# Optimization experiments

Measured on AMD Instinct MI355X. Metric: run time of the kernel, lower is better.

## Reference

```python
import jax, jax.numpy as jnp
import numpy as np
from jax import lax

K_SIZE = 5  # dilated_kernel_size


def dcls_kernel(w, p, k=K_SIZE):
    """Build dense (Cout,Cin,k,k) kernel from DCLS v1 bilinear interpolation.
    w: (Cout,Cin,Kc) weights; p: (2,Cout,Cin,Kc) learnable positions."""
    lim = k // 2
    pos = jnp.clip(p, -lim, lim) + lim          # in [0, k-1]
    i = jnp.floor(pos).astype(jnp.int32)
    r = pos - i                                  # bilinear fractions
    Co, Ci, Kc = w.shape
    co = jnp.arange(Co)[:, None, None]
    ci = jnp.arange(Ci)[None, :, None]
    i1, i2 = i[0], i[1]
    r1, r2 = r[0], r[1]
    # scatter into (k+1)x(k+1) grid so i+1 never goes out of bounds, then trim
    K = jnp.zeros((Co, Ci, k + 1, k + 1), w.dtype)
    K = K.at[co, ci, i1,     i2    ].add(w * (1 - r1) * (1 - r2))
    K = K.at[co, ci, i1 + 1, i2    ].add(w * r1 * (1 - r2))
    K = K.at[co, ci, i1,     i2 + 1].add(w * (1 - r1) * r2)
    K = K.at[co, ci, i1 + 1, i2 + 1].add(w * r1 * r2)
    return K[:, :, :k, :k]


def conv2d(x, K, pad):
    return lax.conv_general_dilated(
        x, K, window_strides=(1, 1), padding=[(pad, pad), (pad, pad)],
        dimension_numbers=('NCHW', 'OIHW', 'NCHW'))


def maxpool2(x):
    return lax.reduce_window(x, -jnp.inf, lax.max, (1, 1, 2, 2), (1, 1, 2, 2), 'VALID')


def setup_inputs() -> dict:
    key = jax.random.key(0)
    ks = jax.random.split(key, 12)
    lim = K_SIZE // 2
    B = 4096
    x = jax.random.normal(ks[0], (B, 1, 28, 28), jnp.float32)
    w1 = jax.random.normal(ks[1], (32, 1, 16), jnp.float32) * 0.2
    p1 = jax.random.uniform(ks[2], (2, 32, 1, 16), jnp.float32, -lim, lim)
    b1 = jnp.zeros((32,), jnp.float32)
    w2 = jax.random.normal(ks[3], (64, 32, 32), jnp.float32) * 0.05
    p2 = jax.random.uniform(ks[4], (2, 64, 32, 32), jnp.float32, -lim, lim)
    b2 = jnp.zeros((64,), jnp.float32)
    fc1_w = jax.random.normal(ks[5], (128, 64 * 7 * 7), jnp.float32) * 0.02
    fc1_b = jnp.zeros((128,), jnp.float32)
    fc2_w = jax.random.normal(ks[6], (10, 128), jnp.float32) * 0.08
    fc2_b = jnp.zeros((10,), jnp.float32)
    return dict(x=x, w1=w1, p1=p1, b1=b1, w2=w2, p2=p2, b2=b2,
                fc1_w=fc1_w, fc1_b=fc1_b, fc2_w=fc2_w, fc2_b=fc2_b)


def reference(x, w1, p1, b1, w2, p2, b2, fc1_w, fc1_b, fc2_w, fc2_b):
    h = conv2d(x, dcls_kernel(w1, p1), pad=2) + b1[None, :, None, None]
    h = maxpool2(jax.nn.relu(h))                       # (B,32,14,14)
    h = conv2d(h, dcls_kernel(w2, p2), pad=2) + b2[None, :, None, None]
    h = maxpool2(jax.nn.relu(h))                       # (B,64,7,7)
    h = h.reshape(-1, 64 * 7 * 7)
    h = jax.nn.relu(h @ fc1_w.T + fc1_b)
    return h @ fc2_w.T + fc2_b                         # (B,10)
```

## Files before the change

### kernel.cpp

```cpp
#include <hip/hip_runtime.h>
#include <hip/hip_bf16.h>

typedef __attribute__((ext_vector_type(8))) short short8;
typedef __attribute__((ext_vector_type(4))) short short4v;
typedef __attribute__((ext_vector_type(4))) float float4v;
typedef __attribute__((ext_vector_type(16))) float float16v;

static __device__ __forceinline__ unsigned short f2bf(float f) {
    unsigned u = __float_as_uint(f);
    unsigned r = (u + 0x7FFF + ((u >> 16) & 1)) >> 16;
    return (unsigned short)r;
}

__global__ __launch_bounds__(256) void prep_all(
    const float* __restrict__ w1, const float* __restrict__ p1,
    const float* __restrict__ w2, const float* __restrict__ p2,
    const float* __restrict__ fc1w,
    unsigned short* __restrict__ K1b,
    unsigned short* __restrict__ Kt,
    unsigned short* __restrict__ w1b) {
    const int blk = blockIdx.x;
    const int t = threadIdx.x;

    if (blk < 8) {
        int cell = blk * 256 + t;
        int co = cell >> 6;
        int k = cell & 63;
        int wr = k >> 3;
        int kx = k & 7;
        float acc = 0.f;
        if (wr < 5 && kx < 5) {
#pragma unroll 8
            for (int kc = 0; kc < 16; ++kc) {
                float wv = w1[co * 16 + kc];
                float pa = p1[co * 16 + kc];
                float pb = p1[512 + co * 16 + kc];
                float pos1 = fminf(fmaxf(pa, -2.f), 2.f) + 2.f;
                float pos2 = fminf(fmaxf(pb, -2.f), 2.f) + 2.f;
                int i1 = (int)floorf(pos1);
                int i2 = (int)floorf(pos2);
                float r1 = pos1 - (float)i1;
                float r2 = pos2 - (float)i2;
                float c = 0.f;
                if (i1 == wr && i2 == kx) c += (1.f - r1) * (1.f - r2);
                if (i1 + 1 == wr && i2 == kx) c += r1 * (1.f - r2);
                if (i1 == wr && i2 + 1 == kx) c += (1.f - r1) * r2;
                if (i1 + 1 == wr && i2 + 1 == kx) c += r1 * r2;
                acc += wv * c;
            }
        }
        K1b[cell] = f2bf(acc);
    } else if (blk < 208) {
        int cell = (blk - 8) * 256 + t;
        int kk = cell >> 11;
        int co = (cell >> 5) & 63;
        int ci = cell & 31;
        int ky = kk / 5;
        int kx = kk - 5 * ky;
        const int base = (co * 32 + ci) * 32;
        float acc = 0.f;
#pragma unroll 8
        for (int kc = 0; kc < 32; ++kc) {
            float wv = w2[base + kc];
            float pa = p2[base + kc];
            float pb = p2[65536 + base + kc];
            float pos1 = fminf(fmaxf(pa, -2.f), 2.f) + 2.f;
            float pos2 = fminf(fmaxf(pb, -2.f), 2.f) + 2.f;
            int i1 = (int)floorf(pos1);
            int i2 = (int)floorf(pos2);
            float r1 = pos1 - (float)i1;
            float r2 = pos2 - (float)i2;
            float c = 0.f;
            if (i1 == ky && i2 == kx) c += (1.f - r1) * (1.f - r2);
            if (i1 + 1 == ky && i2 == kx) c += r1 * (1.f - r2);
            if (i1 == ky && i2 + 1 == kx) c += (1.f - r1) * r2;
            if (i1 + 1 == ky && i2 + 1 == kx) c += r1 * r2;
            acc += wv * c;
        }
        int nt = co >> 5, mq = co & 31;
        int kh2 = ci >> 4, hh = (ci >> 3) & 1, jj = ci & 7;
        Kt[kk * 2048 + nt * 1024 + kh2 * 512 + hh * 256 + mq * 8 + jj] = f2bf(acc);
    } else {
        int i8 = ((blk - 208) * 256 + t) * 8;
        float4 v0 = *(const float4*)(fc1w + i8);
        float4 v1 = *(const float4*)(fc1w + i8 + 4);
        short8 o = {(short)f2bf(v0.x), (short)f2bf(v0.y), (short)f2bf(v0.z),
                    (short)f2bf(v0.w), (short)f2bf(v1.x), (short)f2bf(v1.y),
                    (short)f2bf(v1.z), (short)f2bf(v1.w)};
        *(short8*)(w1b + i8) = o;
    }
}

__global__ __launch_bounds__(256, 4) void fused_conv_mfma(
    const float* __restrict__ x,
    const unsigned short* __restrict__ K1b,
    const unsigned short* __restrict__ Kt,
    const float* __restrict__ b1,
    const float* __restrict__ b2,
    unsigned short* __restrict__ h2) {
    __shared__ __align__(16) unsigned short h1p[18 * 20 * 40];
    __shared__ __align__(16) unsigned short sm4[4 * 29 * 44];
    __shared__ __align__(16) unsigned short sm_xb[784];

    const int b = blockIdx.x;
    const int tid = threadIdx.x;
    const int lane = tid & 63;
    const int wv = tid >> 6;
    const int n16 = lane & 15;
    const int cig = lane >> 4;

    const int yi = 2 * (n16 >> 3) + ((n16 >> 1) & 1);
    const int xi = 2 * ((n16 >> 2) & 1) + (n16 & 1);
    const int pYo = cig >> 1, pXo = cig & 1;

    const int mq = lane & 31;
    const int Qx = mq >> 2;
    const int dy2 = (mq >> 1) & 1;
    const int dx2 = mq & 1;
    const int hh = lane >> 5;

    for (int t = tid; t < 1800; t += 256) ((uint4*)h1p)[t] = uint4{0, 0, 0, 0};
    {
        const float* xb = x + (size_t)b * 784;
        for (int t = tid; t < 784; t += 256) sm_xb[t] = f2bf(xb[t]);
    }
    __syncthreads();

    if (tid < 116) {
        int s = tid / 29;
        int r = tid - s * 29;
        unsigned short* dst = sm4 + (s * 29 + r) * 44;
        bool rok = r < 28;
#pragma unroll
        for (int g2 = 0; g2 < 11; ++g2) {
            short4v v;
#pragma unroll
            for (int e = 0; e < 4; ++e) {
                int c = g2 * 4 + e + s - 4;
                v[e] = (short)((rok && (unsigned)c < 28u) ? sm_xb[r * 28 + c]
                                                          : (unsigned short)0);
            }
            *(short4v*)(dst + g2 * 4) = v;
        }
    }

    short8 bw[2][2];
    float bias1[2], bias2n[2];
#pragma unroll
    for (int cot = 0; cot < 2; ++cot) {
#pragma unroll
        for (int h = 0; h < 2; ++h)
            bw[cot][h] = *(const short8*)(K1b + (cot * 16 + n16) * 64 + h * 32 + cig * 8);
        bias1[cot] = b1[cot * 16 + n16];
    }
#pragma unroll
    for (int nt = 0; nt < 2; ++nt) bias2n[nt] = b2[nt * 32 + mq];

    const int s1 = (xi + 2) & 3;
    const int pb1 = (xi + 2) & ~3;
    const unsigned short* a1base = sm4 + s1 * (29 * 44) + pb1;

    __syncthreads();

    for (int i = 0; i < 13; ++i) {
        int t = wv + 4 * i;
        if (t < 49) {
            int tY = t / 7, tX = t - 7 * tY;
            const unsigned short* ab = a1base + 4 * tX;
            int r0 = 4 * tY + yi - 2 + cig;
            int r1 = r0 + 4;
            int rr0 = ((unsigned)r0 < 28u) ? r0 : 28;
            int rr1 = ((unsigned)r1 < 28u) ? r1 : 28;
            short4v lo0 = *(const short4v*)(ab + rr0 * 44);
            short4v hi0 = *(const short4v*)(ab + rr0 * 44 + 4);
            short4v lo1 = *(const short4v*)(ab + rr1 * 44);
            short4v hi1 = *(const short4v*)(ab + rr1 * 44 + 4);
            short8 af0 = {lo0[0], lo0[1], lo0[2], lo0[3], hi0[0], hi0[1], hi0[2], hi0[3]};
            short8 af1 = {lo1[0], lo1[1], lo1[2], lo1[3], hi1[0], hi1[1], hi1[2], hi1[3]};
            int pY = 2 * tY + pYo, pX = 2 * tX + pXo;
#pragma unroll
            for (int cot = 0; cot < 2; ++cot) {
                float4v acc = {0.f, 0.f, 0.f, 0.f};
                acc = __builtin_amdgcn_mfma_f32_16x16x32_bf16(af0, bw[cot][0], acc, 0, 0, 0);
                acc = __builtin_amdgcn_mfma_f32_16x16x32_bf16(af1, bw[cot][1], acc, 0, 0, 0);
                float v = fmaxf(fmaxf(acc[0], acc[1]), fmaxf(acc[2], acc[3]));
                v = fmaxf(v + bias1[cot], 0.f);
                h1p[((pY + 2) * 20 + (pX + 2)) * 40 + cot * 16 + n16] = f2bf(v);
            }
        }
    }

    int x2 = 2 * Qx + dx2;
    if (x2 > 13) x2 = 13;
    int aoff00, aoff01, aoff10, aoff11;
    int pYv0, pYv1;
    {
        int pY0 = 2 * wv;
        int pY1 = 2 * wv + 1;
        int y20 = 2 * pY0 + dy2; if (y20 > 13) y20 = 13;
        int y21 = 2 * pY1 + dy2; if (y21 > 13) y21 = 13;
        pYv0 = pY0; pYv1 = pY1;
        aoff00 = (y20 * 20 + x2) * 40 + hh * 8;
        aoff01 = aoff00 + 16;
        aoff10 = (y21 * 20 + x2) * 40 + hh * 8;
        aoff11 = aoff10 + 16;
    }
    const unsigned short* KtL = Kt + lane * 8;

    float16v acc00, acc01, acc10, acc11;
#pragma unroll
    for (int e = 0; e < 16; ++e) { acc00[e] = 0.f; acc01[e] = 0.f; acc10[e] = 0.f; acc11[e] = 0.f; }

    __syncthreads();

#pragma unroll 1
    for (int ky = 0; ky < 5; ++ky) {
        const unsigned short* kbase = KtL + ky * 5 * 2048;
        const int sbase = ky * 20 * 40;
#pragma unroll
        for (int kx = 0; kx < 5; ++kx) {
            const unsigned short* kb = kbase + kx * 2048;
            const int soff = sbase + kx * 40;
            short8 wf00 = *(const short8*)(kb);
            short8 wf01 = *(const short8*)(kb + 512);
            short8 wf10 = *(const short8*)(kb + 1024);
            short8 wf11 = *(const short8*)(kb + 1536);
            short8 af00 = *(const short8*)(h1p + aoff00 + soff);
            short8 af01 = *(const short8*)(h1p + aoff01 + soff);
            short8 af10 = *(const short8*)(h1p + aoff10 + soff);
            short8 af11 = *(const short8*)(h1p + aoff11 + soff);
            acc00 = __builtin_amdgcn_mfma_f32_32x32x16_bf16(af00, wf00, acc00, 0, 0, 0);
            acc00 = __builtin_amdgcn_mfma_f32_32x32x16_bf16(af01, wf01, acc00, 0, 0, 0);
            acc01 = __builtin_amdgcn_mfma_f32_32x32x16_bf16(af00, wf10, acc01, 0, 0, 0);
            acc01 = __builtin_amdgcn_mfma_f32_32x32x16_bf16(af01, wf11, acc01, 0, 0, 0);
            acc10 = __builtin_amdgcn_mfma_f32_32x32x16_bf16(af10, wf00, acc10, 0, 0, 0);
            acc10 = __builtin_amdgcn_mfma_f32_32x32x16_bf16(af11, wf01, acc10, 0, 0, 0);
            acc11 = __builtin_amdgcn_mfma_f32_32x32x16_bf16(af10, wf10, acc11, 0, 0, 0);
            acc11 = __builtin_amdgcn_mfma_f32_32x32x16_bf16(af11, wf11, acc11, 0, 0, 0);
        }
    }

    unsigned short* outb = h2 + (size_t)b * 3136;
    if (pYv0 < 7) {
#pragma unroll
        for (int g2 = 0; g2 < 4; ++g2) {
            int pX = 2 * g2 + hh;
            if (pX < 7) {
                float v0 = fmaxf(fmaxf(acc00[4 * g2], acc00[4 * g2 + 1]),
                                 fmaxf(acc00[4 * g2 + 2], acc00[4 * g2 + 3]));
                v0 = fmaxf(v0 + bias2n[0], 0.f);
                outb[mq * 49 + pYv0 * 7 + pX] = f2bf(v0);
                float v1 = fmaxf(fmaxf(acc01[4 * g2], acc01[4 * g2 + 1]),
                                 fmaxf(acc01[4 * g2 + 2], acc01[4 * g2 + 3]));
                v1 = fmaxf(v1 + bias2n[1], 0.f);
                outb[(32 + mq) * 49 + pYv0 * 7 + pX] = f2bf(v1);
            }
        }
    }
    if (pYv1 < 7) {
#pragma unroll
        for (int g2 = 0; g2 < 4; ++g2) {
            int pX = 2 * g2 + hh;
            if (pX < 7) {
                float v0 = fmaxf(fmaxf(acc10[4 * g2], acc10[4 * g2 + 1]),
                                 fmaxf(acc10[4 * g2 + 2], acc10[4 * g2 + 3]));
                v0 = fmaxf(v0 + bias2n[0], 0.f);
                outb[mq * 49 + pYv1 * 7 + pX] = f2bf(v0);
                float v1 = fmaxf(fmaxf(acc11[4 * g2], acc11[4 * g2 + 1]),
                                 fmaxf(acc11[4 * g2 + 2], acc11[4 * g2 + 3]));
                v1 = fmaxf(v1 + bias2n[1], 0.f);
                outb[(32 + mq) * 49 + pYv1 * 7 + pX] = f2bf(v1);
            }
        }
    }
}

__global__ __launch_bounds__(256) void fc1_mfma(
    const unsigned short* __restrict__ A,
    const unsigned short* __restrict__ Wb,
    float* __restrict__ part, size_t PB) {
    __shared__ __align__(16) unsigned short As[64 * 72];
    const int blk = blockIdx.x;
    const int kh = blk % 7;
    const int m0 = (blk / 7) * 64;
    const int tid = threadIdx.x;
    const int wv = tid >> 6;
    const int lane = tid & 63;
    const int n16 = lane & 15;
    const int cig = lane >> 4;

    float4v acc[4][2];
#pragma unroll
    for (int mt = 0; mt < 4; ++mt)
#pragma unroll
        for (int j = 0; j < 2; ++j) acc[mt][j] = float4v{0.f, 0.f, 0.f, 0.f};

    for (int it = 0; it < 7; ++it) {
        int k0 = kh * 448 + it * 64;
        __syncthreads();
#pragma unroll
        for (int i = 0; i < 2; ++i) {
            int p = tid + 256 * i;
            int r = p >> 3, ko = (p & 7) * 8;
            *(short8*)(As + r * 72 + ko) =
                *(const short8*)(A + (size_t)(m0 + r) * 3136 + k0 + ko);
        }
        __syncthreads();
#pragma unroll
        for (int h = 0; h < 2; ++h) {
            short8 af[4];
#pragma unroll
            for (int mt = 0; mt < 4; ++mt)
                af[mt] = *(const short8*)(As + (mt * 16 + n16) * 72 + h * 32 + cig * 8);
            short8 wf[2];
#pragma unroll
            for (int j = 0; j < 2; ++j)
                wf[j] = *(const short8*)(Wb + (size_t)((wv * 2 + j) * 16 + n16) * 3136 +
                                         k0 + h * 32 + cig * 8);
#pragma unroll
            for (int mt = 0; mt < 4; ++mt)
#pragma unroll
                for (int j = 0; j < 2; ++j)
                    acc[mt][j] = __builtin_amdgcn_mfma_f32_16x16x32_bf16(
                        af[mt], wf[j], acc[mt][j], 0, 0, 0);
        }
    }
    float* o = part + (size_t)kh * PB;
#pragma unroll
    for (int mt = 0; mt < 4; ++mt)
#pragma unroll
        for (int j = 0; j < 2; ++j)
#pragma unroll
            for (int r = 0; r < 4; ++r) {
                int row = m0 + mt * 16 + cig * 4 + r;
                o[(size_t)row * 128 + (wv * 2 + j) * 16 + n16] = acc[mt][j][r];
            }
}

__global__ __launch_bounds__(256) void fc2_kernel(
    const float* __restrict__ part, size_t PB,
    const float* __restrict__ fc1b,
    const float* __restrict__ W, const float* __restrict__ bias,
    float* __restrict__ out) {
    __shared__ float smW[10 * 132];
    __shared__ float smB1[128];
    __shared__ float smB[10];
    int t = threadIdx.x;
    for (int i = t; i < 1280; i += 256) {
        int n = i >> 7, k = i & 127;
        smW[n * 132 + k] = W[i];
    }
    if (t < 128) smB1[t] = fc1b[t];
    if (t < 10) smB[t] = bias[t];
    __syncthreads();
    const int r = t >> 3;
    const int q = t & 7;
    const size_t b = (size_t)blockIdx.x * 32 + r;
    const float* pb = part + b * 128 + q * 16;

    float rv[16];
#pragma unroll
    for (int c = 0; c < 4; ++c) {
        float4 s = *(const float4*)(pb + 4 * c);
#pragma unroll
        for (int j = 1; j < 7; ++j) {
            float4 pj = *(const float4*)(pb + (size_t)j * PB + 4 * c);
            s.x += pj.x; s.y += pj.y; s.z += pj.z; s.w += pj.w;
        }
        float4 bv = *(const float4*)(smB1 + q * 16 + 4 * c);
        rv[4 * c + 0] = fmaxf(s.x + bv.x, 0.f);
        rv[4 * c + 1] = fmaxf(s.y + bv.y, 0.f);
        rv[4 * c + 2] = fmaxf(s.z + bv.z, 0.f);
        rv[4 * c + 3] = fmaxf(s.w + bv.w, 0.f);
    }
    float acc[10];
#pragma unroll
    for (int n = 0; n < 10; ++n) {
        const float4* wr = (const float4*)(smW + n * 132 + q * 16);
        float a = 0.f;
#pragma unroll
        for (int c = 0; c < 4; ++c) {
            float4 w = wr[c];
            a += rv[4 * c] * w.x + rv[4 * c + 1] * w.y +
                 rv[4 * c + 2] * w.z + rv[4 * c + 3] * w.w;
        }
        acc[n] = a;
    }
#pragma unroll
    for (int n = 0; n < 10; ++n) {
        acc[n] += __shfl_xor(acc[n], 1);
        acc[n] += __shfl_xor(acc[n], 2);
        acc[n] += __shfl_xor(acc[n], 4);
    }
    if (q == 0) {
#pragma unroll
        for (int n = 0; n < 10; ++n) out[b * 10 + n] = acc[n] + smB[n];
    }
}

extern "C" void kernel_launch(void* const* d_in, const int* in_sizes, int n_in,
                              void* d_out, int out_size, void* d_ws, size_t ws_size,
                              hipStream_t stream) {
    const float* x    = (const float*)d_in[0];
    const float* w1   = (const float*)d_in[1];
    const float* p1   = (const float*)d_in[2];
    const float* b1   = (const float*)d_in[3];
    const float* w2   = (const float*)d_in[4];
    const float* p2   = (const float*)d_in[5];
    const float* b2   = (const float*)d_in[6];
    const float* fc1w = (const float*)d_in[7];
    const float* fc1b = (const float*)d_in[8];
    const float* fc2w = (const float*)d_in[9];
    const float* fc2b = (const float*)d_in[10];
    float* out = (float*)d_out;

    const int B = in_sizes[0] / 784;

    float* ws = (float*)d_ws;
    unsigned short* Kt  = (unsigned short*)ws;
    unsigned short* K1b = (unsigned short*)(ws + 25600);
    unsigned short* w1b = (unsigned short*)(ws + 26624);
    unsigned short* h2b = (unsigned short*)(ws + 227328);
    float* fc1p = ws + 227328 + (size_t)B * 1568;

    prep_all<<<404, 256, 0, stream>>>(w1, p1, w2, p2, fc1w, K1b, Kt, w1b);
    fused_conv_mfma<<<B, 256, 0, stream>>>(x, K1b, Kt, b1, b2, h2b);
    fc1_mfma<<<(B / 64) * 7, 256, 0, stream>>>(h2b, w1b, fc1p, (size_t)B * 128);
    fc2_kernel<<<B / 32, 256, 0, stream>>>(fc1p, (size_t)B * 128,
                                           fc1b, fc2w, fc2b, out);
}
```

Before: 209.7 us.

## Process two images per block in fused conv to reuse conv2 weight loads

```diff
diff --git a/kernel.cpp b/kernel.cpp
--- a/kernel.cpp
+++ b/kernel.cpp
@@ -91,18 +91,19 @@
     }
 }
 
-__global__ __launch_bounds__(256, 4) void fused_conv_mfma(
+__global__ __launch_bounds__(256, 2) void fused_conv2(
     const float* __restrict__ x,
     const unsigned short* __restrict__ K1b,
     const unsigned short* __restrict__ Kt,
     const float* __restrict__ b1,
     const float* __restrict__ b2,
     unsigned short* __restrict__ h2) {
-    __shared__ __align__(16) unsigned short h1p[18 * 20 * 40];
+    __shared__ __align__(16) unsigned short h1pA[18 * 20 * 40];
+    __shared__ __align__(16) unsigned short h1pB[18 * 20 * 40];
     __shared__ __align__(16) unsigned short sm4[4 * 29 * 44];
     __shared__ __align__(16) unsigned short sm_xb[784];
 
-    const int b = blockIdx.x;
+    const int b0 = blockIdx.x * 2;
     const int tid = threadIdx.x;
     const int lane = tid & 63;
     const int wv = tid >> 6;
@@ -119,12 +120,29 @@
     const int dx2 = mq & 1;
     const int hh = lane >> 5;
 
-    for (int t = tid; t < 1800; t += 256) ((uint4*)h1p)[t] = uint4{0, 0, 0, 0};
+    for (int t = tid; t < 1800; t += 256) ((uint4*)h1pA)[t] = uint4{0, 0, 0, 0};
+    for (int t = tid; t < 1800; t += 256) ((uint4*)h1pB)[t] = uint4{0, 0, 0, 0};
     {
-        const float* xb = x + (size_t)b * 784;
+        const float* xb = x + (size_t)b0 * 784;
         for (int t = tid; t < 784; t += 256) sm_xb[t] = f2bf(xb[t]);
     }
     __syncthreads();
+
+    short8 bw[2][2];
+    float bias1[2], bias2n[2];
+#pragma unroll
+    for (int cot = 0; cot < 2; ++cot) {
+#pragma unroll
+        for (int h = 0; h < 2; ++h)
+            bw[cot][h] = *(const short8*)(K1b + (cot * 16 + n16) * 64 + h * 32 + cig * 8);
+        bias1[cot] = b1[cot * 16 + n16];
+    }
+#pragma unroll
+    for (int nt = 0; nt < 2; ++nt) bias2n[nt] = b2[nt * 32 + mq];
+
+    const int s1 = (xi + 2) & 3;
+    const int pb1 = (xi + 2) & ~3;
+    const unsigned short* a1base = sm4 + s1 * (29 * 44) + pb1;
 
     if (tid < 116) {
         int s = tid / 29;
@@ -143,23 +161,6 @@
             *(short4v*)(dst + g2 * 4) = v;
         }
     }
-
-    short8 bw[2][2];
-    float bias1[2], bias2n[2];
-#pragma unroll
-    for (int cot = 0; cot < 2; ++cot) {
-#pragma unroll
-        for (int h = 0; h < 2; ++h)
-            bw[cot][h] = *(const short8*)(K1b + (cot * 16 + n16) * 64 + h * 32 + cig * 8);
-        bias1[cot] = b1[cot * 16 + n16];
-    }
-#pragma unroll
-    for (int nt = 0; nt < 2; ++nt) bias2n[nt] = b2[nt * 32 + mq];
-
-    const int s1 = (xi + 2) & 3;
-    const int pb1 = (xi + 2) & ~3;
-    const unsigned short* a1base = sm4 + s1 * (29 * 44) + pb1;
-
     __syncthreads();
 
     for (int i = 0; i < 13; ++i) {
@@ -185,7 +186,59 @@
                 acc = __builtin_amdgcn_mfma_f32_16x16x32_bf16(af1, bw[cot][1], acc, 0, 0, 0);
                 float v = fmaxf(fmaxf(acc[0], acc[1]), fmaxf(acc[2], acc[3]));
                 v = fmaxf(v + bias1[cot], 0.f);
-                h1p[((pY + 2) * 20 + (pX + 2)) * 40 + cot * 16 + n16] = f2bf(v);
+                h1pA[((pY + 2) * 20 + (pX + 2)) * 40 + cot * 16 + n16] = f2bf(v);
+            }
+        }
+    }
+    {
+        const float* xb = x + ((size_t)b0 + 1) * 784;
+        for (int t = tid; t < 784; t += 256) sm_xb[t] = f2bf(xb[t]);
+    }
+    __syncthreads();
+
+    if (tid < 116) {
+        int s = tid / 29;
+        int r = tid - s * 29;
+        unsigned short* dst = sm4 + (s * 29 + r) * 44;
+        bool rok = r < 28;
+#pragma unroll
+        for (int g2 = 0; g2 < 11; ++g2) {
+            short4v v;
+#pragma unroll
+            for (int e = 0; e < 4; ++e) {
+                int c = g2 * 4 + e + s - 4;
+                v[e] = (short)((rok && (unsigned)c < 28u) ? sm_xb[r * 28 + c]
+                                                          : (unsigned short)0);
+            }
+            *(short4v*)(dst + g2 * 4) = v;
+        }
+    }
+    __syncthreads();
+
+    for (int i = 0; i < 13; ++i) {
+        int t = wv + 4 * i;
+        if (t < 49) {
+            int tY = t / 7, tX = t - 7 * tY;
+            const unsigned short* ab = a1base + 4 * tX;
+            int r0 = 4 * tY + yi - 2 + cig;
+            int r1 = r0 + 4;
+            int rr0 = ((unsigned)r0 < 28u) ? r0 : 28;
+            int rr1 = ((unsigned)r1 < 28u) ? r1 : 28;
+            short4v lo0 = *(const short4v*)(ab + rr0 * 44);
+            short4v hi0 = *(const short4v*)(ab + rr0 * 44 + 4);
+            short4v lo1 = *(const short4v*)(ab + rr1 * 44);
+            short4v hi1 = *(const short4v*)(ab + rr1 * 44 + 4);
+            short8 af0 = {lo0[0], lo0[1], lo0[2], lo0[3], hi0[0], hi0[1], hi0[2], hi0[3]};
+            short8 af1 = {lo1[0], lo1[1], lo1[2], lo1[3], hi1[0], hi1[1], hi1[2], hi1[3]};
+            int pY = 2 * tY + pYo, pX = 2 * tX + pXo;
+#pragma unroll
+            for (int cot = 0; cot < 2; ++cot) {
+                float4v acc = {0.f, 0.f, 0.f, 0.f};
+                acc = __builtin_amdgcn_mfma_f32_16x16x32_bf16(af0, bw[cot][0], acc, 0, 0, 0);
+                acc = __builtin_amdgcn_mfma_f32_16x16x32_bf16(af1, bw[cot][1], acc, 0, 0, 0);
+                float v = fmaxf(fmaxf(acc[0], acc[1]), fmaxf(acc[2], acc[3]));
+                v = fmaxf(v + bias1[cot], 0.f);
+                h1pB[((pY + 2) * 20 + (pX + 2)) * 40 + cot * 16 + n16] = f2bf(v);
             }
         }
     }
@@ -207,9 +260,12 @@
     }
     const unsigned short* KtL = Kt + lane * 8;
 
-    float16v acc00, acc01, acc10, acc11;
-#pragma unroll
-    for (int e = 0; e < 16; ++e) { acc00[e] = 0.f; acc01[e] = 0.f; acc10[e] = 0.f; acc11[e] = 0.f; }
+    float16v aA00, aA01, aA10, aA11, aB00, aB01, aB10, aB11;
+#pragma unroll
+    for (int e = 0; e < 16; ++e) {
+        aA00[e] = 0.f; aA01[e] = 0.f; aA10[e] = 0.f; aA11[e] = 0.f;
+        aB00[e] = 0.f; aB01[e] = 0.f; aB10[e] = 0.f; aB11[e] = 0.f;
+    }
 
     __syncthreads();
 
@@ -225,51 +281,100 @@
             short8 wf01 = *(const short8*)(kb + 512);
             short8 wf10 = *(const short8*)(kb + 1024);
             short8 wf11 = *(const short8*)(kb + 1536);
-            short8 af00 = *(const short8*)(h1p + aoff00 + soff);
-            short8 af01 = *(const short8*)(h1p + aoff01 + soff);
-            short8 af10 = *(const short8*)(h1p + aoff10 + soff);
-            short8 af11 = *(const short8*)(h1p + aoff11 + soff);
-            acc00 = __builtin_amdgcn_mfma_f32_32x32x16_bf16(af00, wf00, acc00, 0, 0, 0);
-            acc00 = __builtin_amdgcn_mfma_f32_32x32x16_bf16(af01, wf01, acc00, 0, 0, 0);
-            acc01 = __builtin_amdgcn_mfma_f32_32x32x16_bf16(af00, wf10, acc01, 0, 0, 0);
-            acc01 = __builtin_amdgcn_mfma_f32_32x32x16_bf16(af01, wf11, acc01, 0, 0, 0);
-            acc10 = __builtin_amdgcn_mfma_f32_32x32x16_bf16(af10, wf00, acc10, 0, 0, 0);
-            acc10 = __builtin_amdgcn_mfma_f32_32x32x16_bf16(af11, wf01, acc10, 0, 0, 0);
-            acc11 = __builtin_amdgcn_mfma_f32_32x32x16_bf16(af10, wf10, acc11, 0, 0, 0);
-            acc11 = __builtin_amdgcn_mfma_f32_32x32x16_bf16(af11, wf11, acc11, 0, 0, 0);
-        }
-    }
-
-    unsigned short* outb = h2 + (size_t)b * 3136;
-    if (pYv0 < 7) {
-#pragma unroll
-        for (int g2 = 0; g2 < 4; ++g2) {
-            int pX = 2 * g2 + hh;
-            if (pX < 7) {
-                float v0 = fmaxf(fmaxf(acc00[4 * g2], acc00[4 * g2 + 1]),
-                                 fmaxf(acc00[4 * g2 + 2], acc00[4 * g2 + 3]));
-                v0 = fmaxf(v0 + bias2n[0], 0.f);
-                outb[mq * 49 + pYv0 * 7 + pX] = f2bf(v0);
-                float v1 = fmaxf(fmaxf(acc01[4 * g2], acc01[4 * g2 + 1]),
-                                 fmaxf(acc01[4 * g2 + 2], acc01[4 * g2 + 3]));
-                v1 = fmaxf(v1 + bias2n[1], 0.f);
-                outb[(32 + mq) * 49 + pYv0 * 7 + pX] = f2bf(v1);
-            }
-        }
-    }
-    if (pYv1 < 7) {
-#pragma unroll
-        for (int g2 = 0; g2 < 4; ++g2) {
-            int pX = 2 * g2 + hh;
-            if (pX < 7) {
-                float v0 = fmaxf(fmaxf(acc10[4 * g2], acc10[4 * g2 + 1]),
-                                 fmaxf(acc10[4 * g2 + 2], acc10[4 * g2 + 3]));
-                v0 = fmaxf(v0 + bias2n[0], 0.f);
-                outb[mq * 49 + pYv1 * 7 + pX] = f2bf(v0);
-                float v1 = fmaxf(fmaxf(acc11[4 * g2], acc11[4 * g2 + 1]),
-                                 fmaxf(acc11[4 * g2 + 2], acc11[4 * g2 + 3]));
-                v1 = fmaxf(v1 + bias2n[1], 0.f);
-                outb[(32 + mq) * 49 + pYv1 * 7 + pX] = f2bf(v1);
+            short8 fA00 = *(const short8*)(h1pA + aoff00 + soff);
+            short8 fA01 = *(const short8*)(h1pA + aoff01 + soff);
+            short8 fA10 = *(const short8*)(h1pA + aoff10 + soff);
+            short8 fA11 = *(const short8*)(h1pA + aoff11 + soff);
+            short8 fB00 = *(const short8*)(h1pB + aoff00 + soff);
+            short8 fB01 = *(const short8*)(h1pB + aoff01 + soff);
+            short8 fB10 = *(const short8*)(h1pB + aoff10 + soff);
+            short8 fB11 = *(const short8*)(h1pB + aoff11 + soff);
+            aA00 = __builtin_amdgcn_mfma_f32_32x32x16_bf16(fA00, wf00, aA00, 0, 0, 0);
+            aA00 = __builtin_amdgcn_mfma_f32_32x32x16_bf16(fA01, wf01, aA00, 0, 0, 0);
+            aA01 = __builtin_amdgcn_mfma_f32_32x32x16_bf16(fA00, wf10, aA01, 0, 0, 0);
+            aA01 = __builtin_amdgcn_mfma_f32_32x32x16_bf16(fA01, wf11, aA01, 0, 0, 0);
+            aA10 = __builtin_amdgcn_mfma_f32_32x32x16_bf16(fA10, wf00, aA10, 0, 0, 0);
+            aA10 = __builtin_amdgcn_mfma_f32_32x32x16_bf16(fA11, wf01, aA10, 0, 0, 0);
+            aA11 = __builtin_amdgcn_mfma_f32_32x32x16_bf16(fA10, wf10, aA11, 0, 0, 0);
+            aA11 = __builtin_amdgcn_mfma_f32_32x32x16_bf16(fA11, wf11, aA11, 0, 0, 0);
+            aB00 = __builtin_amdgcn_mfma_f32_32x32x16_bf16(fB00, wf00, aB00, 0, 0, 0);
+            aB00 = __builtin_amdgcn_mfma_f32_32x32x16_bf16(fB01, wf01, aB00, 0, 0, 0);
+            aB01 = __builtin_amdgcn_mfma_f32_32x32x16_bf16(fB00, wf10, aB01, 0, 0, 0);
+            aB01 = __builtin_amdgcn_mfma_f32_32x32x16_bf16(fB01, wf11, aB01, 0, 0, 0);
+            aB10 = __builtin_amdgcn_mfma_f32_32x32x16_bf16(fB10, wf00, aB10, 0, 0, 0);
+            aB10 = __builtin_amdgcn_mfma_f32_32x32x16_bf16(fB11, wf01, aB10, 0, 0, 0);
+            aB11 = __builtin_amdgcn_mfma_f32_32x32x16_bf16(fB10, wf10, aB11, 0, 0, 0);
+            aB11 = __builtin_amdgcn_mfma_f32_32x32x16_bf16(fB11, wf11, aB11, 0, 0, 0);
+        }
+    }
+
+    {
+        unsigned short* outb = h2 + (size_t)b0 * 3136;
+        if (pYv0 < 7) {
+#pragma unroll
+            for (int g2 = 0; g2 < 4; ++g2) {
+                int pX = 2 * g2 + hh;
+                if (pX < 7) {
+                    float v0 = fmaxf(fmaxf(aA00[4 * g2], aA00[4 * g2 + 1]),
+                                     fmaxf(aA00[4 * g2 + 2], aA00[4 * g2 + 3]));
+                    v0 = fmaxf(v0 + bias2n[0], 0.f);
+                    outb[mq * 49 + pYv0 * 7 + pX] = f2bf(v0);
+                    float v1 = fmaxf(fmaxf(aA01[4 * g2], aA01[4 * g2 + 1]),
+                                     fmaxf(aA01[4 * g2 + 2], aA01[4 * g2 + 3]));
+                    v1 = fmaxf(v1 + bias2n[1], 0.f);
+                    outb[(32 + mq) * 49 + pYv0 * 7 + pX] = f2bf(v1);
+                }
+            }
+        }
+        if (pYv1 < 7) {
+#pragma unroll
+            for (int g2 = 0; g2 < 4; ++g2) {
+                int pX = 2 * g2 + hh;
+                if (pX < 7) {
+                    float v0 = fmaxf(fmaxf(aA10[4 * g2], aA10[4 * g2 + 1]),
+                                     fmaxf(aA10[4 * g2 + 2], aA10[4 * g2 + 3]));
+                    v0 = fmaxf(v0 + bias2n[0], 0.f);
+                    outb[mq * 49 + pYv1 * 7 + pX] = f2bf(v0);
+                    float v1 = fmaxf(fmaxf(aA11[4 * g2], aA11[4 * g2 + 1]),
+                                     fmaxf(aA11[4 * g2 + 2], aA11[4 * g2 + 3]));
+                    v1 = fmaxf(v1 + bias2n[1], 0.f);
+                    outb[(32 + mq) * 49 + pYv1 * 7 + pX] = f2bf(v1);
+                }
+            }
+        }
+    }
+    {
+        unsigned short* outb = h2 + ((size_t)b0 + 1) * 3136;
+        if (pYv0 < 7) {
+#pragma unroll
+            for (int g2 = 0; g2 < 4; ++g2) {
+                int pX = 2 * g2 + hh;
+                if (pX < 7) {
+                    float v0 = fmaxf(fmaxf(aB00[4 * g2], aB00[4 * g2 + 1]),
+                                     fmaxf(aB00[4 * g2 + 2], aB00[4 * g2 + 3]));
+                    v0 = fmaxf(v0 + bias2n[0], 0.f);
+                    outb[mq * 49 + pYv0 * 7 + pX] = f2bf(v0);
+                    float v1 = fmaxf(fmaxf(aB01[4 * g2], aB01[4 * g2 + 1]),
+                                     fmaxf(aB01[4 * g2 + 2], aB01[4 * g2 + 3]));
+                    v1 = fmaxf(v1 + bias2n[1], 0.f);
+                    outb[(32 + mq) * 49 + pYv0 * 7 + pX] = f2bf(v1);
+                }
+            }
+        }
+        if (pYv1 < 7) {
+#pragma unroll
+            for (int g2 = 0; g2 < 4; ++g2) {
+                int pX = 2 * g2 + hh;
+                if (pX < 7) {
+                    float v0 = fmaxf(fmaxf(aB10[4 * g2], aB10[4 * g2 + 1]),
+                                     fmaxf(aB10[4 * g2 + 2], aB10[4 * g2 + 3]));
+                    v0 = fmaxf(v0 + bias2n[0], 0.f);
+                    outb[mq * 49 + pYv1 * 7 + pX] = f2bf(v0);
+                    float v1 = fmaxf(fmaxf(aB11[4 * g2], aB11[4 * g2 + 1]),
+                                     fmaxf(aB11[4 * g2 + 2], aB11[4 * g2 + 3]));
+                    v1 = fmaxf(v1 + bias2n[1], 0.f);
+                    outb[(32 + mq) * 49 + pYv1 * 7 + pX] = f2bf(v1);
+                }
             }
         }
     }
@@ -424,7 +529,7 @@
     float* fc1p = ws + 227328 + (size_t)B * 1568;
 
     prep_all<<<404, 256, 0, stream>>>(w1, p1, w2, p2, fc1w, K1b, Kt, w1b);
-    fused_conv_mfma<<<B, 256, 0, stream>>>(x, K1b, Kt, b1, b2, h2b);
+    fused_conv2<<<B / 2, 256, 0, stream>>>(x, K1b, Kt, b1, b2, h2b);
     fc1_mfma<<<(B / 64) * 7, 256, 0, stream>>>(h2b, w1b, fc1p, (size_t)B * 128);
     fc2_kernel<<<B / 32, 256, 0, stream>>>(fc1p, (size_t)B * 128,
                                            fc1b, fc2w, fc2b, out);
```

New measurement: 220.0 us. 4.9% more time.

## Fuse fc1 and fc2 into one kernel without split-K partials

Applied to the files above, without the earlier changes.

```diff
diff --git a/kernel.cpp b/kernel.cpp
--- a/kernel.cpp
+++ b/kernel.cpp
@@ -275,126 +275,92 @@
     }
 }
 
-__global__ __launch_bounds__(256) void fc1_mfma(
+__global__ __launch_bounds__(256) void fused_fc(
     const unsigned short* __restrict__ A,
     const unsigned short* __restrict__ Wb,
-    float* __restrict__ part, size_t PB) {
-    __shared__ __align__(16) unsigned short As[64 * 72];
-    const int blk = blockIdx.x;
-    const int kh = blk % 7;
-    const int m0 = (blk / 7) * 64;
+    const float* __restrict__ fc1b,
+    const float* __restrict__ W2,
+    const float* __restrict__ b2,
+    float* __restrict__ out) {
+    __shared__ __align__(16) unsigned short As[16 * 72];
+    __shared__ float Hs[16][132];
+    __shared__ float smW[10 * 132];
+    __shared__ float smB[10];
+
+    const int m0 = blockIdx.x * 16;
     const int tid = threadIdx.x;
     const int wv = tid >> 6;
     const int lane = tid & 63;
     const int n16 = lane & 15;
     const int cig = lane >> 4;
 
-    float4v acc[4][2];
-#pragma unroll
-    for (int mt = 0; mt < 4; ++mt)
-#pragma unroll
-        for (int j = 0; j < 2; ++j) acc[mt][j] = float4v{0.f, 0.f, 0.f, 0.f};
-
-    for (int it = 0; it < 7; ++it) {
-        int k0 = kh * 448 + it * 64;
+    for (int i = tid; i < 1280; i += 256) {
+        int n = i >> 7, k = i & 127;
+        smW[n * 132 + k] = W2[i];
+    }
+    if (tid < 10) smB[tid] = b2[tid];
+
+    float4v acc[2];
+    acc[0] = float4v{0.f, 0.f, 0.f, 0.f};
+    acc[1] = float4v{0.f, 0.f, 0.f, 0.f};
+
+    for (int it = 0; it < 49; ++it) {
+        const int k0 = it * 64;
         __syncthreads();
-#pragma unroll
-        for (int i = 0; i < 2; ++i) {
-            int p = tid + 256 * i;
-            int r = p >> 3, ko = (p & 7) * 8;
+        if (tid < 128) {
+            int r = tid >> 3, ko = (tid & 7) * 8;
             *(short8*)(As + r * 72 + ko) =
                 *(const short8*)(A + (size_t)(m0 + r) * 3136 + k0 + ko);
         }
         __syncthreads();
 #pragma unroll
         for (int h = 0; h < 2; ++h) {
-            short8 af[4];
-#pragma unroll
-            for (int mt = 0; mt < 4; ++mt)
-                af[mt] = *(const short8*)(As + (mt * 16 + n16) * 72 + h * 32 + cig * 8);
-            short8 wf[2];
-#pragma unroll
-            for (int j = 0; j < 2; ++j)
-                wf[j] = *(const short8*)(Wb + (size_t)((wv * 2 + j) * 16 + n16) * 3136 +
-                                         k0 + h * 32 + cig * 8);
-#pragma unroll
-            for (int mt = 0; mt < 4; ++mt)
-#pragma unroll
-                for (int j = 0; j < 2; ++j)
-                    acc[mt][j] = __builtin_amdgcn_mfma_f32_16x16x32_bf16(
-                        af[mt], wf[j], acc[mt][j], 0, 0, 0);
-        }
-    }
-    float* o = part + (size_t)kh * PB;
-#pragma unroll
-    for (int mt = 0; mt < 4; ++mt)
-#pragma unroll
-        for (int j = 0; j < 2; ++j)
-#pragma unroll
-            for (int r = 0; r < 4; ++r) {
-                int row = m0 + mt * 16 + cig * 4 + r;
-                o[(size_t)row * 128 + (wv * 2 + j) * 16 + n16] = acc[mt][j][r];
-            }
-}
-
-__global__ __launch_bounds__(256) void fc2_kernel(
-    const float* __restrict__ part, size_t PB,
-    const float* __restrict__ fc1b,
-    const float* __restrict__ W, const float* __restrict__ bias,
-    float* __restrict__ out) {
-    __shared__ float smW[10 * 132];
-    __shared__ float smB1[128];
-    __shared__ float smB[10];
-    int t = threadIdx.x;
-    for (int i = t; i < 1280; i += 256) {
-        int n = i >> 7, k = i & 127;
-        smW[n * 132 + k] = W[i];
-    }
-    if (t < 128) smB1[t] = fc1b[t];
-    if (t < 10) smB[t] = bias[t];
-    __syncthreads();
-    const int r = t >> 3;
-    const int q = t & 7;
-    const size_t b = (size_t)blockIdx.x * 32 + r;
-    const float* pb = part + b * 128 + q * 16;
-
-    float rv[16];
-#pragma unroll
-    for (int c = 0; c < 4; ++c) {
-        float4 s = *(const float4*)(pb + 4 * c);
-#pragma unroll
-        for (int j = 1; j < 7; ++j) {
-            float4 pj = *(const float4*)(pb + (size_t)j * PB + 4 * c);
-            s.x += pj.x; s.y += pj.y; s.z += pj.z; s.w += pj.w;
-        }
-        float4 bv = *(const float4*)(smB1 + q * 16 + 4 * c);
-        rv[4 * c + 0] = fmaxf(s.x + bv.x, 0.f);
-        rv[4 * c + 1] = fmaxf(s.y + bv.y, 0.f);
-        rv[4 * c + 2] = fmaxf(s.z + bv.z, 0.f);
-        rv[4 * c + 3] = fmaxf(s.w + bv.w, 0.f);
-    }
-    float acc[10];
+            short8 af = *(const short8*)(As + n16 * 72 + h * 32 + cig * 8);
+#pragma unroll
+            for (int j = 0; j < 2; ++j) {
+                short8 wf = *(const short8*)(Wb + (size_t)((wv * 2 + j) * 16 + n16) * 3136 +
+                                             k0 + h * 32 + cig * 8);
+                acc[j] = __builtin_amdgcn_mfma_f32_16x16x32_bf16(af, wf, acc[j], 0, 0, 0);
+            }
+        }
+    }
+
+    __syncthreads();
+#pragma unroll
+    for (int j = 0; j < 2; ++j) {
+        int col = (wv * 2 + j) * 16 + n16;
+        float bb = fc1b[col];
+#pragma unroll
+        for (int r = 0; r < 4; ++r)
+            Hs[cig * 4 + r][col] = fmaxf(acc[j][r] + bb, 0.f);
+    }
+    __syncthreads();
+
+    const int row = tid >> 4;
+    const int q = tid & 15;
+    float rv[8];
+#pragma unroll
+    for (int c = 0; c < 8; ++c) rv[c] = Hs[row][q * 8 + c];
+    float facc[10];
 #pragma unroll
     for (int n = 0; n < 10; ++n) {
-        const float4* wr = (const float4*)(smW + n * 132 + q * 16);
+        const float* wr = smW + n * 132 + q * 8;
         float a = 0.f;
 #pragma unroll
-        for (int c = 0; c < 4; ++c) {
-            float4 w = wr[c];
-            a += rv[4 * c] * w.x + rv[4 * c + 1] * w.y +
-                 rv[4 * c + 2] * w.z + rv[4 * c + 3] * w.w;
-        }
-        acc[n] = a;
+        for (int c = 0; c < 8; ++c) a += rv[c] * wr[c];
+        facc[n] = a;
     }
 #pragma unroll
     for (int n = 0; n < 10; ++n) {
-        acc[n] += __shfl_xor(acc[n], 1);
-        acc[n] += __shfl_xor(acc[n], 2);
-        acc[n] += __shfl_xor(acc[n], 4);
+        facc[n] += __shfl_xor(facc[n], 1);
+        facc[n] += __shfl_xor(facc[n], 2);
+        facc[n] += __shfl_xor(facc[n], 4);
+        facc[n] += __shfl_xor(facc[n], 8);
     }
     if (q == 0) {
 #pragma unroll
-        for (int n = 0; n < 10; ++n) out[b * 10 + n] = acc[n] + smB[n];
+        for (int n = 0; n < 10; ++n)
+            out[(size_t)(m0 + row) * 10 + n] = facc[n] + smB[n];
     }
 }
 
@@ -421,11 +387,8 @@
     unsigned short* K1b = (unsigned short*)(ws + 25600);
     unsigned short* w1b = (unsigned short*)(ws + 26624);
     unsigned short* h2b = (unsigned short*)(ws + 227328);
-    float* fc1p = ws + 227328 + (size_t)B * 1568;
 
     prep_all<<<404, 256, 0, stream>>>(w1, p1, w2, p2, fc1w, K1b, Kt, w1b);
     fused_conv_mfma<<<B, 256, 0, stream>>>(x, K1b, Kt, b1, b2, h2b);
-    fc1_mfma<<<(B / 64) * 7, 256, 0, stream>>>(h2b, w1b, fc1p, (size_t)B * 128);
-    fc2_kernel<<<B / 32, 256, 0, stream>>>(fc1p, (size_t)B * 128,
-                                           fc1b, fc2w, fc2b, out);
-}
+    fused_fc<<<B / 16, 256, 0, stream>>>(h2b, w1b, fc1b, fc2w, fc2b, out);
+}
```

After: 246.6 us. 17.6% more time.
